# Kernel optimization log

Measured on AMD Instinct MI355X. Metric: run time of the kernel, lower is better.

Reference implementation:

```python
import jax, jax.numpy as jnp
import numpy as np

D_IN = 1024
D_OUT = 1024
NUM_HEADS = 16
HEAD_DIM = D_OUT // NUM_HEADS
SEQ = 2048
BATCH = 4


def setup_inputs() -> dict:
    key = jax.random.key(0)
    ks = jax.random.split(key, 6)
    s_in = 1.0 / np.sqrt(D_IN)
    s_out = 1.0 / np.sqrt(D_OUT)
    return {
        "inputs": jax.random.normal(ks[0], (BATCH, SEQ, D_IN), dtype=jnp.float32),
        # nn.Linear stores weight as [out, in]; y = x @ W.T
        "W_q": jax.random.uniform(ks[1], (D_OUT, D_IN), jnp.float32, -s_in, s_in),
        "W_k": jax.random.uniform(ks[2], (D_OUT, D_IN), jnp.float32, -s_in, s_in),
        "W_v": jax.random.uniform(ks[3], (D_OUT, D_IN), jnp.float32, -s_in, s_in),
        "W_o": jax.random.uniform(ks[4], (D_OUT, D_OUT), jnp.float32, -s_out, s_out),
        "b_o": jax.random.uniform(ks[5], (D_OUT,), jnp.float32, -s_out, s_out),
    }


def reference(inputs, W_q, W_k, W_v, W_o, b_o):
    B, T, _ = inputs.shape
    # projections: [B, T, d_out] -> [B, H, T, hd]
    def split_heads(x):
        return x.reshape(B, T, NUM_HEADS, HEAD_DIM).transpose(0, 2, 1, 3)

    Q = split_heads(inputs @ W_q.T)
    K = split_heads(inputs @ W_k.T)
    V = split_heads(inputs @ W_v.T)

    # [B, H, T, T] causal attention scores
    scores = jnp.einsum("bhqd,bhkd->bhqk", Q, K)
    causal = jnp.tril(jnp.ones((T, T), dtype=bool))  # True = keep
    scores = jnp.where(causal, scores, -jnp.inf)
    weights = jax.nn.softmax(scores / np.sqrt(HEAD_DIM), axis=-1)
    # dropout p=0.0 (eval mode): identity

    ctx = jnp.einsum("bhqk,bhkd->bhqd", weights, V)
    ctx = ctx.transpose(0, 2, 1, 3).reshape(B, T, D_OUT)
    return ctx @ W_o.T + b_o
```

## Files before the change

kernel.cpp:

```cpp
#include <hip/hip_runtime.h>
#include <cstdint>
#include <cstddef>

#define D_MODEL 1024
#define SEQQ    2048
#define NBATCH  4
#define NHEAD   16
#define HDIM    64
#define MTOT    (NBATCH * SEQQ)

typedef __attribute__((ext_vector_type(8))) short short8;
typedef __attribute__((ext_vector_type(4))) float floatx4;
typedef unsigned short u16;

__device__ __forceinline__ u16 f2bf(float f) {
  union { float f; uint32_t u; } a; a.f = f;
  uint32_t u = a.u;
  u += 0x7fffu + ((u >> 16) & 1u);
  return (u16)(u >> 16);
}

__device__ __forceinline__ floatx4 mfma16(short8 a, short8 b, floatx4 c) {
  return __builtin_amdgcn_mfma_f32_16x16x32_bf16(a, b, c, 0, 0, 0);
}

__device__ __forceinline__ void load_lds16(const void* g, void* l) {
  __builtin_amdgcn_global_load_lds(
      (const __attribute__((address_space(1))) uint32_t*)g,
      (__attribute__((address_space(3))) uint32_t*)l, 16, 0, 0);
}

__global__ __launch_bounds__(256) void k_cast_all(
    const float* __restrict__ X, const float* __restrict__ w0,
    const float* __restrict__ w1, const float* __restrict__ w2,
    const float* __restrict__ w3,
    u16* __restrict__ xb, u16* __restrict__ y0, u16* __restrict__ y1,
    u16* __restrict__ y2, u16* __restrict__ y3) {
  const int bx = blockIdx.x;
  const float* src; u16* dst; int i;
  if (bx < 8192) {
    src = X; dst = xb; i = (bx * 256 + threadIdx.x) * 4;
  } else {
    const int w = (bx - 8192) >> 10;
    src = (w == 0) ? w0 : (w == 1) ? w1 : (w == 2) ? w2 : w3;
    dst = (w == 0) ? y0 : (w == 1) ? y1 : (w == 2) ? y2 : y3;
    i = (((bx - 8192) & 1023) * 256 + threadIdx.x) * 4;
  }
  float4 v = *(const float4*)(src + i);
  ushort4 o;
  o.x = f2bf(v.x); o.y = f2bf(v.y); o.z = f2bf(v.z); o.w = f2bf(v.w);
  *(ushort4*)(dst + i) = o;
}

__global__ __launch_bounds__(256) void k_gemm_bt(
    const u16* __restrict__ A,
    const u16* __restrict__ B0, const u16* __restrict__ B1, const u16* __restrict__ B2,
    void* __restrict__ C0, void* __restrict__ C1, u16* __restrict__ VtOut,
    const float* __restrict__ bias, int M, int N, int K, int f32out, float ascaleQ) {
  __shared__ __align__(16) u16 As[128 * 64];
  __shared__ __align__(16) u16 Bs[128 * 64];
  const int tid = threadIdx.x;
  const int lane = tid & 63, wave = tid >> 6;
  const int quad = lane >> 4, l15 = lane & 15;
  const int m0 = blockIdx.y * 128, n0 = blockIdx.x * 128;
  const int wr = wave >> 1, wc = wave & 1;
  const u16* Bm = (blockIdx.z == 0) ? B0 : (blockIdx.z == 1 ? B1 : B2);
  void* Cm = (blockIdx.z == 0) ? C0 : C1;
  const float ascale = (blockIdx.z == 0) ? ascaleQ : 1.0f;

  floatx4 acc[4][4];
#pragma unroll
  for (int i = 0; i < 4; ++i)
#pragma unroll
    for (int j = 0; j < 4; ++j) acc[i][j] = (floatx4){0.f, 0.f, 0.f, 0.f};

  const int srow = tid >> 3;
  const int scolx = ((tid & 7) * 8) ^ ((srow & 7) * 8);
  const u16* Ag = A + (size_t)(m0 + srow) * K + scolx;
  const u16* Bg = Bm + (size_t)(n0 + srow) * K + scolx;

  for (int kt = 0; kt < K; kt += 64) {
    __syncthreads();
#pragma unroll
    for (int p = 0; p < 4; ++p) {
      load_lds16(Ag + (size_t)(p * 32) * K + kt, &As[p * 2048 + wave * 512]);
      load_lds16(Bg + (size_t)(p * 32) * K + kt, &Bs[p * 2048 + wave * 512]);
    }
    __syncthreads();

    short8 af[2][4], bfg[2][4];
#pragma unroll
    for (int ks = 0; ks < 2; ++ks) {
      const int kkx = (ks * 32 + quad * 8) ^ ((l15 & 7) * 8);
#pragma unroll
      for (int i = 0; i < 4; ++i) {
        af[ks][i]  = *(const short8*)&As[(wr * 64 + i * 16 + l15) * 64 + kkx];
        bfg[ks][i] = *(const short8*)&Bs[(wc * 64 + i * 16 + l15) * 64 + kkx];
      }
    }
#pragma unroll
    for (int ks = 0; ks < 2; ++ks)
#pragma unroll
      for (int mi = 0; mi < 4; ++mi)
#pragma unroll
        for (int ni = 0; ni < 4; ++ni)
          acc[mi][ni] = mfma16(af[ks][mi], bfg[ks][ni], acc[mi][ni]);
  }

  if (blockIdx.z == 2) {
#pragma unroll
    for (int mi = 0; mi < 4; ++mi) {
#pragma unroll
      for (int ni = 0; ni < 4; ++ni) {
        const int row = m0 + wr * 64 + mi * 16 + quad * 4;
        const int col = n0 + wc * 64 + ni * 16 + l15;
        const int b = row >> 11, t = row & 2047;
        const int h = col >> 6, d = col & 63;
        ushort4 pk;
        pk.x = f2bf(acc[mi][ni][0]); pk.y = f2bf(acc[mi][ni][1]);
        pk.z = f2bf(acc[mi][ni][2]); pk.w = f2bf(acc[mi][ni][3]);
        *(ushort4*)(VtOut + (((size_t)(b * 16 + h) * 64 + d) * SEQQ + t)) = pk;
      }
    }
    return;
  }
#pragma unroll
  for (int mi = 0; mi < 4; ++mi) {
#pragma unroll
    for (int ni = 0; ni < 4; ++ni) {
      const int row = m0 + wr * 64 + mi * 16 + quad * 4;
      const int col = n0 + wc * 64 + ni * 16 + l15;
      const float bv = bias ? bias[col] : 0.f;
#pragma unroll
      for (int r = 0; r < 4; ++r) {
        const float v = acc[mi][ni][r] * ascale + bv;
        if (f32out) ((float*)Cm)[(size_t)(row + r) * N + col] = v;
        else        ((u16*)Cm)[(size_t)(row + r) * N + col] = f2bf(v);
      }
    }
  }
}

__device__ __forceinline__ short8 mk8(uint32_t a, uint32_t b, uint32_t c, uint32_t d) {
  union { uint32_t u[4]; short8 s; } t;
  t.u[0] = a; t.u[1] = b; t.u[2] = c; t.u[3] = d;
  return t.s;
}

__device__ __forceinline__ void softmax_reg(
    const floatx4 (&st)[4], float& lp, uint32_t (&w)[4][2]) {
#pragma unroll
  for (int ni = 0; ni < 4; ++ni) {
    const float p0 = __builtin_amdgcn_exp2f(st[ni][0]);
    const float p1 = __builtin_amdgcn_exp2f(st[ni][1]);
    const float p2 = __builtin_amdgcn_exp2f(st[ni][2]);
    const float p3 = __builtin_amdgcn_exp2f(st[ni][3]);
    lp += (p0 + p1) + (p2 + p3);
    w[ni][0] = __builtin_amdgcn_perm(__float_as_uint(p1), __float_as_uint(p0), 0x07060302u);
    w[ni][1] = __builtin_amdgcn_perm(__float_as_uint(p3), __float_as_uint(p2), 0x07060302u);
  }
}

__device__ __forceinline__ short8 pf_prep(const uint32_t (&w)[4][2], int kc) {
  uint32_t y0 = w[2 * kc][0], z0 = w[2 * kc + 1][0];
  asm("v_permlane32_swap_b32 %0, %1" : "+v"(y0), "+v"(z0));
  asm("v_permlane16_swap_b32 %0, %1" : "+v"(y0), "+v"(z0));
  uint32_t y1 = w[2 * kc][1], z1 = w[2 * kc + 1][1];
  asm("v_permlane32_swap_b32 %0, %1" : "+v"(y1), "+v"(z1));
  asm("v_permlane16_swap_b32 %0, %1" : "+v"(y1), "+v"(z1));
  return mk8(y0, y1, z0, z1);
}

__global__ __launch_bounds__(512) void k_attn(
    const u16* __restrict__ Q, const u16* __restrict__ Kg,
    const u16* __restrict__ Vt, u16* __restrict__ O) {
  __shared__ __align__(16) u16 Ks[2][128 * 64];
  __shared__ __align__(16) u16 Vs[2][64 * 128];
  const int tid = threadIdx.x, lane = tid & 63, wave = tid >> 6;
  const int quad = lane >> 4, l15 = lane & 15;

  const int lin = blockIdx.x;
  const int c = lin & 255, k2 = lin >> 8;
  const int g = k2 ? (7 - (c & 7)) : (c & 7);
  const int bh = (c >> 3) | (k2 << 5);
  const int b = bh >> 4, h = bh & 15;

  const int wgrp = wave >> 2, wsub = wave & 3;
  const int a = 2 * g + wgrp;
  const int qwA = 64 * a + wsub * 16;
  const int qwB = SEQQ - 64 * (a + 1) + wsub * 16;
  const int nT = 16 - g;
  const int uB = 31 - a;

  const u16* kbase = Kg + (size_t)(b * SEQQ) * D_MODEL + h * HDIM;
  const u16* vbase = Vt + (size_t)bh * (HDIM * SEQQ);

  const int krow = tid >> 3;
  const int kcol = ((tid & 7) * 8) ^ ((krow & 7) * 8);
  const int vrow = tid >> 4;
  const int vslot = tid & 15;
  const int vcol = (vslot >> 3) * 64 + (((vslot & 7) ^ (vrow & 7)) * 8);

#define STAGE_KV(tt, buf)                                                           \
  {                                                                                 \
    const int kt_ = (tt) * 128;                                                     \
    load_lds16(kbase + (size_t)(kt_ + krow) * D_MODEL + kcol,                       \
               &Ks[buf][wave * 512]);                                               \
    load_lds16(kbase + (size_t)(kt_ + 64 + krow) * D_MODEL + kcol,                  \
               &Ks[buf][4096 + wave * 512]);                                        \
    load_lds16(vbase + (size_t)vrow * SEQQ + kt_ + vcol,                            \
               &Vs[buf][wave * 512]);                                               \
    load_lds16(vbase + (size_t)(32 + vrow) * SEQQ + kt_ + vcol,                     \
               &Vs[buf][4096 + wave * 512]);                                        \
  }

  STAGE_KV(0, 0);

  short8 qfA[2], qfB[2];
  {
    const u16* qa = Q + (size_t)(b * SEQQ + qwA + l15) * D_MODEL + h * HDIM;
    const u16* qb = Q + (size_t)(b * SEQQ + qwB + l15) * D_MODEL + h * HDIM;
#pragma unroll
    for (int ks = 0; ks < 2; ++ks) {
      qfA[ks] = *(const short8*)(qa + ks * 32 + quad * 8);
      qfB[ks] = *(const short8*)(qb + ks * 32 + quad * 8);
    }
  }

  floatx4 accA[4], accB[4];
  float lAp = 0.f, lBp = 0.f;
#pragma unroll
  for (int i = 0; i < 4; ++i) {
    accA[i] = (floatx4){0.f, 0.f, 0.f, 0.f};
    accB[i] = (floatx4){0.f, 0.f, 0.f, 0.f};
  }

  for (int t = 0; t < nT; ++t) {
    const int cur = t & 1;
    __syncthreads();
    if (t + 1 < nT) STAGE_KV(t + 1, cur ^ 1);

#pragma unroll
    for (int sub = 0; sub < 2; ++sub) {
      const int u = 2 * t + sub;
      const bool doA = (u <= a);
      const bool doB = (u <= uB);

      short8 kf[4][2];
#pragma unroll
      for (int ni = 0; ni < 4; ++ni)
#pragma unroll
        for (int ks = 0; ks < 2; ++ks)
          kf[ni][ks] = *(const short8*)&Ks[cur][(sub * 64 + ni * 16 + l15) * 64 +
                                               ((ks * 32 + quad * 8) ^ ((l15 & 7) * 8))];
      short8 vf[2][4];
#pragma unroll
      for (int kc = 0; kc < 2; ++kc)
#pragma unroll
        for (int di = 0; di < 4; ++di)
          vf[kc][di] = *(const short8*)&Vs[cur][(di * 16 + l15) * 128 + sub * 64 +
                                               ((kc * 32 + quad * 8) ^ ((l15 & 7) * 8))];

      uint32_t wA[4][2], wB[4][2];
      if (doA) {
        floatx4 st[4];
        __builtin_amdgcn_s_setprio(1);
#pragma unroll
        for (int ni = 0; ni < 4; ++ni) {
          floatx4 s = (floatx4){0.f, 0.f, 0.f, 0.f};
          s = mfma16(kf[ni][0], qfA[0], s);
          s = mfma16(kf[ni][1], qfA[1], s);
          st[ni] = s;
        }
        __builtin_amdgcn_s_setprio(0);
        if (u == a) {
          const int qg = qwA + l15;
#pragma unroll
          for (int ni = 0; ni < 4; ++ni) {
            const int kg = u * 64 + ni * 16 + quad * 4;
#pragma unroll
            for (int r = 0; r < 4; ++r)
              if (kg + r > qg) st[ni][r] = -1e30f;
          }
        }
        softmax_reg(st, lAp, wA);
      }
      if (doB) {
        floatx4 st[4];
        __builtin_amdgcn_s_setprio(1);
#pragma unroll
        for (int ni = 0; ni < 4; ++ni) {
          floatx4 s = (floatx4){0.f, 0.f, 0.f, 0.f};
          s = mfma16(kf[ni][0], qfB[0], s);
          s = mfma16(kf[ni][1], qfB[1], s);
          st[ni] = s;
        }
        __builtin_amdgcn_s_setprio(0);
        if (u == uB) {
          const int qg = qwB + l15;
#pragma unroll
          for (int ni = 0; ni < 4; ++ni) {
            const int kg = u * 64 + ni * 16 + quad * 4;
#pragma unroll
            for (int r = 0; r < 4; ++r)
              if (kg + r > qg) st[ni][r] = -1e30f;
          }
        }
        softmax_reg(st, lBp, wB);
      }
#pragma unroll
      for (int kc = 0; kc < 2; ++kc) {
        if (doA) {
          const short8 pfA = pf_prep(wA, kc);
          __builtin_amdgcn_s_setprio(1);
#pragma unroll
          for (int di = 0; di < 4; ++di)
            accA[di] = mfma16(pfA, vf[kc][di], accA[di]);
          __builtin_amdgcn_s_setprio(0);
        }
        if (doB) {
          const short8 pfB = pf_prep(wB, kc);
          __builtin_amdgcn_s_setprio(1);
#pragma unroll
          for (int di = 0; di < 4; ++di)
            accB[di] = mfma16(pfB, vf[kc][di], accB[di]);
          __builtin_amdgcn_s_setprio(0);
        }
      }
    }
  }

  lAp += __shfl_xor(lAp, 16); lAp += __shfl_xor(lAp, 32);
  lBp += __shfl_xor(lBp, 16); lBp += __shfl_xor(lBp, 32);

  {
    u16* orow = O + (size_t)(b * SEQQ + qwA + quad * 4) * D_MODEL + h * HDIM + l15;
#pragma unroll
    for (int r = 0; r < 4; ++r) {
      const float inv = 1.0f / __shfl(lAp, quad * 4 + r, 16);
#pragma unroll
      for (int di = 0; di < 4; ++di)
        orow[(size_t)r * D_MODEL + di * 16] = f2bf(accA[di][r] * inv);
    }
  }
  {
    u16* orow = O + (size_t)(b * SEQQ + qwB + quad * 4) * D_MODEL + h * HDIM + l15;
#pragma unroll
    for (int r = 0; r < 4; ++r) {
      const float inv = 1.0f / __shfl(lBp, quad * 4 + r, 16);
#pragma unroll
      for (int di = 0; di < 4; ++di)
        orow[(size_t)r * D_MODEL + di * 16] = f2bf(accB[di][r] * inv);
    }
  }
}

extern "C" void kernel_launch(void* const* d_in, const int* in_sizes, int n_in,
                              void* d_out, int out_size, void* d_ws, size_t ws_size,
                              hipStream_t stream) {
  const float* X  = (const float*)d_in[0];
  const float* Wq = (const float*)d_in[1];
  const float* Wk = (const float*)d_in[2];
  const float* Wv = (const float*)d_in[3];
  const float* Wo = (const float*)d_in[4];
  const float* bo = (const float*)d_in[5];
  float* out = (float*)d_out;

  u16* ws = (u16*)d_ws;
  const size_t NE = (size_t)MTOT * D_MODEL;
  u16* Xb  = ws;
  u16* Qb  = Xb + NE;
  u16* Kb  = Qb + NE;
  u16* Vt  = Kb + NE;
  u16* Cb  = Vt + NE;
  u16* Wqb = Cb + NE;
  u16* Wkb = Wqb + (size_t)D_MODEL * D_MODEL;
  u16* Wvb = Wkb + (size_t)D_MODEL * D_MODEL;
  u16* Wob = Wvb + (size_t)D_MODEL * D_MODEL;

  const float SCL2E = 0.18033688f;

  k_cast_all<<<12288, 256, 0, stream>>>(X, Wq, Wk, Wv, Wo, Xb, Wqb, Wkb, Wvb, Wob);

  k_gemm_bt<<<dim3(D_MODEL / 128, MTOT / 128, 3), 256, 0, stream>>>(
      Xb, Wqb, Wkb, Wvb, Qb, Kb, Vt, nullptr, MTOT, D_MODEL, D_MODEL, 0, SCL2E);

  k_attn<<<512, 512, 0, stream>>>(Qb, Kb, Vt, Cb);

  k_gemm_bt<<<dim3(D_MODEL / 128, MTOT / 128, 1), 256, 0, stream>>>(
      Cb, Wob, Wob, Wob, out, out, nullptr, bo, MTOT, D_MODEL, D_MODEL, 1, 1.0f);
}
```

Baseline: 271.4 us.

## Double-buffer GEMM LDS tiles and swizzle block order for locality

The projection GEMM kernel now keeps two LDS buffers and issues the global-to-LDS loads for the next K tile before computing on the current one, removing one barrier per iteration. The grid is also flattened into a 1-D block index that is remapped so consecutive blocks share the same N tile across different M tiles, which is meant to improve L2 reuse of weights. LDS use doubles to 64KB per block, which may lower occupancy. Correctness of the single barrier depends on the async LDS loads being complete before they are read.

After: 248.3 us. 8.5% less time.

```diff
diff --git a/kernel.cpp b/kernel.cpp
--- a/kernel.cpp
+++ b/kernel.cpp
@@ -57,12 +57,16 @@
     const u16* __restrict__ B0, const u16* __restrict__ B1, const u16* __restrict__ B2,
     void* __restrict__ C0, void* __restrict__ C1, u16* __restrict__ VtOut,
     const float* __restrict__ bias, int M, int N, int K, int f32out, float ascaleQ) {
-  __shared__ __align__(16) u16 As[128 * 64];
-  __shared__ __align__(16) u16 Bs[128 * 64];
+  __shared__ __align__(16) u16 As[2][128 * 64];
+  __shared__ __align__(16) u16 Bs[2][128 * 64];
   const int tid = threadIdx.x;
   const int lane = tid & 63, wave = tid >> 6;
   const int quad = lane >> 4, l15 = lane & 15;
-  const int m0 = blockIdx.y * 128, n0 = blockIdx.x * 128;
+
+  const int bx = blockIdx.x;
+  const int swz = (bx & 7) * 64 + (bx >> 3);
+  const int m0 = (swz >> 3) * 128, n0 = (swz & 7) * 128;
+
   const int wr = wave >> 1, wc = wave & 1;
   const u16* Bm = (blockIdx.z == 0) ? B0 : (blockIdx.z == 1 ? B1 : B2);
   void* Cm = (blockIdx.z == 0) ? C0 : C1;
@@ -79,14 +83,23 @@
   const u16* Ag = A + (size_t)(m0 + srow) * K + scolx;
   const u16* Bg = Bm + (size_t)(n0 + srow) * K + scolx;
 
-  for (int kt = 0; kt < K; kt += 64) {
+#define STAGE_AB(tt, buf)                                                            \
+  {                                                                                  \
+    const int kk_ = (tt) * 64;                                                       \
+    _Pragma("unroll")                                                                \
+    for (int p = 0; p < 4; ++p) {                                                    \
+      load_lds16(Ag + (size_t)(p * 32) * K + kk_, &As[buf][p * 2048 + wave * 512]);  \
+      load_lds16(Bg + (size_t)(p * 32) * K + kk_, &Bs[buf][p * 2048 + wave * 512]);  \
+    }                                                                                \
+  }
+
+  const int nIt = K / 64;
+  STAGE_AB(0, 0);
+
+  for (int it = 0; it < nIt; ++it) {
+    const int cur = it & 1;
     __syncthreads();
-#pragma unroll
-    for (int p = 0; p < 4; ++p) {
-      load_lds16(Ag + (size_t)(p * 32) * K + kt, &As[p * 2048 + wave * 512]);
-      load_lds16(Bg + (size_t)(p * 32) * K + kt, &Bs[p * 2048 + wave * 512]);
-    }
-    __syncthreads();
+    if (it + 1 < nIt) STAGE_AB(it + 1, cur ^ 1);
 
     short8 af[2][4], bfg[2][4];
 #pragma unroll
@@ -94,8 +107,8 @@
       const int kkx = (ks * 32 + quad * 8) ^ ((l15 & 7) * 8);
 #pragma unroll
       for (int i = 0; i < 4; ++i) {
-        af[ks][i]  = *(const short8*)&As[(wr * 64 + i * 16 + l15) * 64 + kkx];
-        bfg[ks][i] = *(const short8*)&Bs[(wc * 64 + i * 16 + l15) * 64 + kkx];
+        af[ks][i]  = *(const short8*)&As[cur][(wr * 64 + i * 16 + l15) * 64 + kkx];
+        bfg[ks][i] = *(const short8*)&Bs[cur][(wc * 64 + i * 16 + l15) * 64 + kkx];
       }
     }
 #pragma unroll
@@ -106,6 +119,7 @@
         for (int ni = 0; ni < 4; ++ni)
           acc[mi][ni] = mfma16(af[ks][mi], bfg[ks][ni], acc[mi][ni]);
   }
+#undef STAGE_AB
 
   if (blockIdx.z == 2) {
 #pragma unroll
@@ -382,11 +396,11 @@
 
   k_cast_all<<<12288, 256, 0, stream>>>(X, Wq, Wk, Wv, Wo, Xb, Wqb, Wkb, Wvb, Wob);
 
-  k_gemm_bt<<<dim3(D_MODEL / 128, MTOT / 128, 3), 256, 0, stream>>>(
+  k_gemm_bt<<<dim3(512, 1, 3), 256, 0, stream>>>(
       Xb, Wqb, Wkb, Wvb, Qb, Kb, Vt, nullptr, MTOT, D_MODEL, D_MODEL, 0, SCL2E);
 
   k_attn<<<512, 512, 0, stream>>>(Qb, Kb, Vt, Cb);
 
-  k_gemm_bt<<<dim3(D_MODEL / 128, MTOT / 128, 1), 256, 0, stream>>>(
+  k_gemm_bt<<<dim3(512, 1, 1), 256, 0, stream>>>(
       Cb, Wob, Wob, Wob, out, out, nullptr, bo, MTOT, D_MODEL, D_MODEL, 1, 1.0f);
 }
```
